# Kernel tuning notes

Hardware: AMD Instinct MI355X
Metric: run time of the kernel (lower is better)

## Reference

```python
import jax, jax.numpy as jnp
import numpy as np

RES = 128          # voxel grid resolution
N = 262144
C_IN = 64
C_OUT = 64
K = 3              # kernel size -> 27 offsets


def _build_rulebook(coords, res, k):
    """Submanifold sparse conv rulebook (stride=1, padding=k//2).
    Returns in_idx, out_idx [K^3, N] int32 and mask [K^3, N] float32."""
    n = coords.shape[0]
    lin = (coords[:, 0] * res + coords[:, 1]) * res + coords[:, 2]
    order = np.argsort(lin)
    sorted_lin = lin[order]
    r = k // 2
    in_idx, out_idx, mask = [], [], []
    for dx in range(-r, r + 1):
        for dy in range(-r, r + 1):
            for dz in range(-r, r + 1):
                nb = coords + np.array([dx, dy, dz])
                inb = np.all((nb >= 0) & (nb < res), axis=1)
                nlin = (nb[:, 0] * res + nb[:, 1]) * res + nb[:, 2]
                pos = np.searchsorted(sorted_lin, nlin)
                pos_c = np.clip(pos, 0, n - 1)
                found = inb & (sorted_lin[pos_c] == nlin)
                in_idx.append(np.where(found, order[pos_c], 0))
                out_idx.append(np.where(found, np.arange(n), 0))
                mask.append(found.astype(np.float32))
    return (np.asarray(in_idx, np.int32), np.asarray(out_idx, np.int32),
            np.asarray(mask, np.float32))


def setup_inputs() -> dict:
    rng = np.random.default_rng(0)
    lin = rng.choice(RES ** 3, size=N, replace=False)
    coords = np.stack([lin // (RES * RES), (lin // RES) % RES, lin % RES], axis=1)
    in_idx, out_idx, mask = _build_rulebook(coords, RES, K)

    key = jax.random.key(0)
    kf, kw, kb = jax.random.split(key, 3)
    feats = jax.random.normal(kf, (N, C_IN), dtype=jnp.float32)
    weight = jax.random.normal(kw, (K ** 3, C_IN, C_OUT), dtype=jnp.float32) * 0.02
    bias = jax.random.normal(kb, (C_OUT,), dtype=jnp.float32) * 0.02
    return {
        "feats": feats,
        "weight": weight,
        "bias": bias,
        "in_idx": jnp.asarray(in_idx),
        "out_idx": jnp.asarray(out_idx),
        "mask": jnp.asarray(mask),
    }


def reference(feats, weight, bias, in_idx, out_idx, mask):
    # gather -> GEMM -> scatter per kernel offset (27 fixed offsets)
    n = feats.shape[0]
    out = jnp.tile(bias[None, :], (n, 1))  # [N, C_out]
    for k in range(weight.shape[0]):
        g = feats[in_idx[k]] * mask[k][:, None]   # [N, C_in], zeros where no pair
        out = out.at[out_idx[k]].add(g @ weight[k])  # invalid rows add zeros at row 0
    return out
```

## Files before the change

### kernel.cpp

```cpp
#include <hip/hip_runtime.h>

#define CIN  64
#define COUT 64
#define KVOL 27

typedef __attribute__((ext_vector_type(8))) short bf16x8;
typedef __attribute__((ext_vector_type(4))) float f32x4;

union U4H8 { uint4 u; bf16x8 h; };

static __device__ __forceinline__ unsigned short f2bf(float x) {
    union { float f; unsigned int u; } v; v.f = x;
    return (unsigned short)((v.u + 0x7FFFu + ((v.u >> 16) & 1u)) >> 16);
}

__global__ __launch_bounds__(256) void pack_w(const float* __restrict__ W,
                                              unsigned short* __restrict__ wf) {
    int t = blockIdx.x * 256 + threadIdx.x;
    if (t >= KVOL * 8 * 64) return;
    int lane  = t & 63;
    int frag  = (t >> 6) & 7;
    int k     = t >> 9;
    int kh    = frag >> 2, nt = frag & 3;
    int col   = nt * 16 + (lane & 15);
    int kbase = kh * 32 + (lane >> 4) * 8;
    const float* src = W + (size_t)k * (CIN * COUT) + (size_t)kbase * COUT + col;
    unsigned int pk[4];
    #pragma unroll
    for (int j = 0; j < 4; ++j) {
        unsigned int lo = f2bf(src[(2 * j) * COUT]);
        unsigned int hi = f2bf(src[(2 * j + 1) * COUT]);
        pk[j] = lo | (hi << 16);
    }
    *reinterpret_cast<uint4*>(wf + (size_t)t * 8) = make_uint4(pk[0], pk[1], pk[2], pk[3]);
}

__global__ __launch_bounds__(256) void cvt_feats(const float* __restrict__ f,
                                                 uint4* __restrict__ o, int total8) {
    int t = blockIdx.x * 256 + threadIdx.x;
    if (t < total8) {
        const float4* p = reinterpret_cast<const float4*>(f) + 2 * (size_t)t;
        float4 a = p[0], b = p[1];
        unsigned int u0 = (unsigned int)f2bf(a.x) | ((unsigned int)f2bf(a.y) << 16);
        unsigned int u1 = (unsigned int)f2bf(a.z) | ((unsigned int)f2bf(a.w) << 16);
        unsigned int u2 = (unsigned int)f2bf(b.x) | ((unsigned int)f2bf(b.y) << 16);
        unsigned int u3 = (unsigned int)f2bf(b.z) | ((unsigned int)f2bf(b.w) << 16);
        o[t] = make_uint4(u0, u1, u2, u3);
    } else if (t < total8 + 8) {
        o[t] = make_uint4(0u, 0u, 0u, 0u);
    }
}

__global__ __launch_bounds__(128) void spconv_mfma64(
    const char* __restrict__ fbf,
    const uint4* __restrict__ wf4,
    const float* __restrict__ bias,
    const int*   __restrict__ in_idx,
    const float* __restrict__ mask,
    float* __restrict__ out, int n)
{
    const int tid  = threadIdx.x;
    const int lane = tid & 63;
    const int wv   = tid >> 6;
    const int rloc = lane & 15;
    const int grp  = lane >> 4;
    const int row0 = blockIdx.x * 128 + wv * 64;

    __shared__ uint4 lds_w[2][512];

    f32x4 acc[4][4];
    #pragma unroll
    for (int nt = 0; nt < 4; ++nt) {
        float b = bias[nt * 16 + rloc];
        f32x4 v = {b, b, b, b};
        acc[0][nt] = v; acc[1][nt] = v; acc[2][nt] = v; acc[3][nt] = v;
    }

    int rowt[4];
    #pragma unroll
    for (int t = 0; t < 4; ++t) rowt[t] = row0 + 16 * t + rloc;

    const unsigned zoff = (unsigned)n * 128u;

    int idxb[4]; float mskb[4];
    #pragma unroll
    for (int t = 0; t < 4; ++t) { idxb[t] = in_idx[rowt[t]]; mskb[t] = mask[rowt[t]]; }

    unsigned offs[2][4];
    #pragma unroll
    for (int t = 0; t < 4; ++t)
        offs[0][t] = (mskb[t] != 0.0f) ? (unsigned)idxb[t] * 128u : zoff;

    #pragma unroll
    for (int t = 0; t < 4; ++t) {
        idxb[t] = in_idx[(size_t)n + rowt[t]];
        mskb[t] = mask[(size_t)n + rowt[t]];
    }

    U4H8 a[2][4][2];
    #pragma unroll
    for (int t = 0; t < 4; ++t) {
        const uint4* p = reinterpret_cast<const uint4*>(fbf + offs[0][t]) + grp;
        a[0][t][0].u = p[0];
        a[0][t][1].u = p[4];
    }

    lds_w[0][tid]       = wf4[tid];
    lds_w[0][tid + 128] = wf4[tid + 128];
    lds_w[0][tid + 256] = wf4[tid + 256];
    lds_w[0][tid + 384] = wf4[tid + 384];
    __syncthreads();

    #pragma unroll
    for (int k = 0; k < KVOL; ++k) {
        const int cur = k & 1;
        const int nxt = cur ^ 1;

        uint4 w0, w1, w2, w3;
        if (k + 1 < KVOL) {
            const uint4* s = wf4 + (size_t)(k + 1) * 512;
            w0 = s[tid]; w1 = s[tid + 128]; w2 = s[tid + 256]; w3 = s[tid + 384];
        }

        if (k + 1 < KVOL) {
            #pragma unroll
            for (int t = 0; t < 4; ++t)
                offs[nxt][t] = (mskb[t] != 0.0f) ? (unsigned)idxb[t] * 128u : zoff;
        }

        if (k + 2 < KVOL) {
            const size_t kb = (size_t)(k + 2) * n;
            #pragma unroll
            for (int t = 0; t < 4; ++t) {
                idxb[t] = in_idx[kb + rowt[t]];
                mskb[t] = mask[kb + rowt[t]];
            }
        }

        if (k + 1 < KVOL) {
            #pragma unroll
            for (int t = 0; t < 4; ++t) {
                const uint4* p = reinterpret_cast<const uint4*>(fbf + offs[nxt][t]) + grp;
                a[nxt][t][0].u = p[0];
                a[nxt][t][1].u = p[4];
            }
        }

        U4H8 bf[2][4];
        #pragma unroll
        for (int kh = 0; kh < 2; ++kh)
            #pragma unroll
            for (int ntl = 0; ntl < 4; ++ntl)
                bf[kh][ntl].u = lds_w[cur][(kh * 4 + ntl) * 64 + lane];

        #pragma unroll
        for (int t = 0; t < 4; ++t)
            #pragma unroll
            for (int ntl = 0; ntl < 4; ++ntl) {
                acc[t][ntl] = __builtin_amdgcn_mfma_f32_16x16x32_bf16(a[cur][t][0].h, bf[0][ntl].h, acc[t][ntl], 0, 0, 0);
                acc[t][ntl] = __builtin_amdgcn_mfma_f32_16x16x32_bf16(a[cur][t][1].h, bf[1][ntl].h, acc[t][ntl], 0, 0, 0);
            }

        if (k + 1 < KVOL) {
            lds_w[nxt][tid]       = w0;
            lds_w[nxt][tid + 128] = w1;
            lds_w[nxt][tid + 256] = w2;
            lds_w[nxt][tid + 384] = w3;
            __syncthreads();
        }
    }

    #pragma unroll
    for (int t = 0; t < 4; ++t)
        #pragma unroll
        for (int ntl = 0; ntl < 4; ++ntl)
            #pragma unroll
            for (int r = 0; r < 4; ++r) {
                int orow = row0 + 16 * t + grp * 4 + r;
                out[(size_t)orow * COUT + ntl * 16 + rloc] = acc[t][ntl][r];
            }
}

static __device__ __forceinline__ bf16x8 cvt8(float4 a, float4 b, float m) {
    bf16x8 r;
    r[0] = (short)f2bf(a.x * m); r[1] = (short)f2bf(a.y * m);
    r[2] = (short)f2bf(a.z * m); r[3] = (short)f2bf(a.w * m);
    r[4] = (short)f2bf(b.x * m); r[5] = (short)f2bf(b.y * m);
    r[6] = (short)f2bf(b.z * m); r[7] = (short)f2bf(b.w * m);
    return r;
}

__global__ __launch_bounds__(256) void spconv_mfma_f32(
    const float* __restrict__ feats,
    const unsigned short* __restrict__ wf,
    const float* __restrict__ bias,
    const int*   __restrict__ in_idx,
    const float* __restrict__ mask,
    float* __restrict__ out, int n)
{
    const int tid  = threadIdx.x;
    const int lane = tid & 63;
    const int wv   = tid >> 6;
    const int rloc = lane & 15;
    const int grp  = lane >> 4;
    const int row0 = blockIdx.x * 128 + wv * 32;

    __shared__ uint4 lds_w[2][512];

    f32x4 acc[2][4];
    #pragma unroll
    for (int nt = 0; nt < 4; ++nt) {
        float b = bias[nt * 16 + rloc];
        f32x4 v = {b, b, b, b};
        acc[0][nt] = v; acc[1][nt] = v;
    }

    const uint4* wf4 = reinterpret_cast<const uint4*>(wf);
    lds_w[0][tid]       = wf4[tid];
    lds_w[0][tid + 256] = wf4[tid + 256];
    __syncthreads();

    const int rowA = row0 + rloc;
    const int rowB = rowA + 16;

    for (int koff = 0; koff < KVOL; ++koff) {
        const int cur = koff & 1;
        uint4 w0, w1;
        const bool pf = (koff + 1 < KVOL);
        if (pf) {
            const uint4* s = wf4 + (size_t)(koff + 1) * 512;
            w0 = s[tid]; w1 = s[tid + 256];
        }

        const size_t kb = (size_t)koff * n;
        const int   idxA = in_idx[kb + rowA];
        const float mA   = mask[kb + rowA];
        const int   idxB = in_idx[kb + rowB];
        const float mB   = mask[kb + rowB];

        const float4* fA = reinterpret_cast<const float4*>(feats + (size_t)idxA * CIN + grp * 8);
        const float4* fB = reinterpret_cast<const float4*>(feats + (size_t)idxB * CIN + grp * 8);
        float4 a0 = fA[0], a1 = fA[1], a2 = fA[8], a3 = fA[9];
        float4 c0 = fB[0], c1 = fB[1], c2 = fB[8], c3 = fB[9];

        bf16x8 aA0 = cvt8(a0, a1, mA), aA1 = cvt8(a2, a3, mA);
        bf16x8 aB0 = cvt8(c0, c1, mB), aB1 = cvt8(c2, c3, mB);

        U4H8 bf[2][4];
        #pragma unroll
        for (int kh = 0; kh < 2; ++kh)
            #pragma unroll
            for (int nt = 0; nt < 4; ++nt)
                bf[kh][nt].u = lds_w[cur][(kh * 4 + nt) * 64 + lane];

        #pragma unroll
        for (int nt = 0; nt < 4; ++nt) {
            acc[0][nt] = __builtin_amdgcn_mfma_f32_16x16x32_bf16(aA0, bf[0][nt].h, acc[0][nt], 0, 0, 0);
            acc[0][nt] = __builtin_amdgcn_mfma_f32_16x16x32_bf16(aA1, bf[1][nt].h, acc[0][nt], 0, 0, 0);
            acc[1][nt] = __builtin_amdgcn_mfma_f32_16x16x32_bf16(aB0, bf[0][nt].h, acc[1][nt], 0, 0, 0);
            acc[1][nt] = __builtin_amdgcn_mfma_f32_16x16x32_bf16(aB1, bf[1][nt].h, acc[1][nt], 0, 0, 0);
        }

        if (pf) {
            lds_w[cur ^ 1][tid]       = w0;
            lds_w[cur ^ 1][tid + 256] = w1;
        }
        __syncthreads();
    }

    #pragma unroll
    for (int t = 0; t < 2; ++t)
        #pragma unroll
        for (int nt = 0; nt < 4; ++nt)
            #pragma unroll
            for (int r = 0; r < 4; ++r) {
                int orow = row0 + t * 16 + grp * 4 + r;
                out[(size_t)orow * COUT + nt * 16 + rloc] = acc[t][nt][r];
            }
}

extern "C" void kernel_launch(void* const* d_in, const int* in_sizes, int n_in,
                              void* d_out, int out_size, void* d_ws, size_t ws_size,
                              hipStream_t stream)
{
    const float* feats  = (const float*)d_in[0];
    const float* weight = (const float*)d_in[1];
    const float* bias   = (const float*)d_in[2];
    const int*   in_idx = (const int*)  d_in[3];
    const float* mask   = (const float*)d_in[5];
    float* out = (float*)d_out;

    const int n = in_sizes[0] / CIN;

    const size_t WF_BYTES  = (size_t)KVOL * 8 * 64 * 16;
    const size_t FBF_BYTES = (size_t)(n + 1) * CIN * 2;

    unsigned short* wf = (unsigned short*)d_ws;
    const int packN = KVOL * 8 * 64;
    pack_w<<<(packN + 255) / 256, 256, 0, stream>>>(weight, wf);

    if (ws_size >= WF_BYTES + FBF_BYTES) {
        char* fbf = (char*)d_ws + WF_BYTES;
        const int total8 = n * 8;
        cvt_feats<<<(total8 + 8 + 255) / 256, 256, 0, stream>>>(feats, (uint4*)fbf, total8);
        spconv_mfma64<<<n / 128, 128, 0, stream>>>(fbf, (const uint4*)wf, bias,
                                                   in_idx, mask, out, n);
    } else {
        spconv_mfma_f32<<<n / 128, 256, 0, stream>>>(feats, wf, bias,
                                                     in_idx, mask, out, n);
    }
}
```

Before: 99.13 us.

## Split output channels across waves and load weights directly from global memory

Each block now covers 64 rows with 4 waves, and each wave computes one 16-column slice of the output instead of all 64 columns. Weight fragments are read per wave straight from global memory (L2-cached) and double-buffered in registers, which removes the LDS staging and the per-offset __syncthreads. Index and mask prefetching moves one stage further ahead. In exchange every wave gathers the same feature rows, so gather traffic per output row is four times higher (relying on cache hits), but there are fewer accumulators per thread and likely higher occupancy.

```diff
diff --git a/kernel.cpp b/kernel.cpp
--- a/kernel.cpp
+++ b/kernel.cpp
@@ -51,7 +51,7 @@
     }
 }
 
-__global__ __launch_bounds__(128) void spconv_mfma64(
+__global__ __launch_bounds__(256) void spconv_nsplit(
     const char* __restrict__ fbf,
     const uint4* __restrict__ wf4,
     const float* __restrict__ bias,
@@ -64,16 +64,13 @@
     const int wv   = tid >> 6;
     const int rloc = lane & 15;
     const int grp  = lane >> 4;
-    const int row0 = blockIdx.x * 128 + wv * 64;
-
-    __shared__ uint4 lds_w[2][512];
-
-    f32x4 acc[4][4];
-    #pragma unroll
-    for (int nt = 0; nt < 4; ++nt) {
-        float b = bias[nt * 16 + rloc];
-        f32x4 v = {b, b, b, b};
-        acc[0][nt] = v; acc[1][nt] = v; acc[2][nt] = v; acc[3][nt] = v;
+    const int row0 = blockIdx.x * 64;
+
+    f32x4 acc[4];
+    {
+        const float bb = bias[wv * 16 + rloc];
+        f32x4 v = {bb, bb, bb, bb};
+        acc[0] = v; acc[1] = v; acc[2] = v; acc[3] = v;
     }
 
     int rowt[4];
@@ -82,103 +79,77 @@
 
     const unsigned zoff = (unsigned)n * 128u;
 
-    int idxb[4]; float mskb[4];
-    #pragma unroll
-    for (int t = 0; t < 4; ++t) { idxb[t] = in_idx[rowt[t]]; mskb[t] = mask[rowt[t]]; }
-
-    unsigned offs[2][4];
-    #pragma unroll
-    for (int t = 0; t < 4; ++t)
-        offs[0][t] = (mskb[t] != 0.0f) ? (unsigned)idxb[t] * 128u : zoff;
-
+    int idxb[2][4]; float mskb[2][4];
+    #pragma unroll
+    for (int t = 0; t < 4; ++t) { idxb[0][t] = in_idx[rowt[t]];            mskb[0][t] = mask[rowt[t]]; }
+    #pragma unroll
+    for (int t = 0; t < 4; ++t) { idxb[1][t] = in_idx[(size_t)n + rowt[t]]; mskb[1][t] = mask[(size_t)n + rowt[t]]; }
+
+    U4H8 a[2][4][2];
+    U4H8 b[2][2];
+    {
+        unsigned o[4];
+        #pragma unroll
+        for (int t = 0; t < 4; ++t)
+            o[t] = (mskb[0][t] != 0.0f) ? (unsigned)idxb[0][t] * 128u : zoff;
+        #pragma unroll
+        for (int t = 0; t < 4; ++t) {
+            const uint4* p = reinterpret_cast<const uint4*>(fbf + o[t]) + grp;
+            a[0][t][0].u = p[0];
+            a[0][t][1].u = p[4];
+        }
+        b[0][0].u = wf4[(0 * 8 + 0 * 4 + wv) * 64 + lane];
+        b[0][1].u = wf4[(0 * 8 + 1 * 4 + wv) * 64 + lane];
+    }
     #pragma unroll
     for (int t = 0; t < 4; ++t) {
-        idxb[t] = in_idx[(size_t)n + rowt[t]];
-        mskb[t] = mask[(size_t)n + rowt[t]];
-    }
-
-    U4H8 a[2][4][2];
-    #pragma unroll
-    for (int t = 0; t < 4; ++t) {
-        const uint4* p = reinterpret_cast<const uint4*>(fbf + offs[0][t]) + grp;
-        a[0][t][0].u = p[0];
-        a[0][t][1].u = p[4];
-    }
-
-    lds_w[0][tid]       = wf4[tid];
-    lds_w[0][tid + 128] = wf4[tid + 128];
-    lds_w[0][tid + 256] = wf4[tid + 256];
-    lds_w[0][tid + 384] = wf4[tid + 384];
-    __syncthreads();
+        idxb[0][t] = in_idx[(size_t)2 * n + rowt[t]];
+        mskb[0][t] = mask[(size_t)2 * n + rowt[t]];
+    }
 
     #pragma unroll
     for (int k = 0; k < KVOL; ++k) {
         const int cur = k & 1;
         const int nxt = cur ^ 1;
 
-        uint4 w0, w1, w2, w3;
         if (k + 1 < KVOL) {
-            const uint4* s = wf4 + (size_t)(k + 1) * 512;
-            w0 = s[tid]; w1 = s[tid + 128]; w2 = s[tid + 256]; w3 = s[tid + 384];
-        }
-
-        if (k + 1 < KVOL) {
+            unsigned o[4];
             #pragma unroll
             for (int t = 0; t < 4; ++t)
-                offs[nxt][t] = (mskb[t] != 0.0f) ? (unsigned)idxb[t] * 128u : zoff;
-        }
-
-        if (k + 2 < KVOL) {
-            const size_t kb = (size_t)(k + 2) * n;
+                o[t] = (mskb[nxt][t] != 0.0f) ? (unsigned)idxb[nxt][t] * 128u : zoff;
             #pragma unroll
             for (int t = 0; t < 4; ++t) {
-                idxb[t] = in_idx[kb + rowt[t]];
-                mskb[t] = mask[kb + rowt[t]];
-            }
-        }
-
-        if (k + 1 < KVOL) {
-            #pragma unroll
-            for (int t = 0; t < 4; ++t) {
-                const uint4* p = reinterpret_cast<const uint4*>(fbf + offs[nxt][t]) + grp;
+                const uint4* p = reinterpret_cast<const uint4*>(fbf + o[t]) + grp;
                 a[nxt][t][0].u = p[0];
                 a[nxt][t][1].u = p[4];
             }
-        }
-
-        U4H8 bf[2][4];
-        #pragma unroll
-        for (int kh = 0; kh < 2; ++kh)
-            #pragma unroll
-            for (int ntl = 0; ntl < 4; ++ntl)
-                bf[kh][ntl].u = lds_w[cur][(kh * 4 + ntl) * 64 + lane];
-
-        #pragma unroll
-        for (int t = 0; t < 4; ++t)
-            #pragma unroll
-            for (int ntl = 0; ntl < 4; ++ntl) {
-                acc[t][ntl] = __builtin_amdgcn_mfma_f32_16x16x32_bf16(a[cur][t][0].h, bf[0][ntl].h, acc[t][ntl], 0, 0, 0);
-                acc[t][ntl] = __builtin_amdgcn_mfma_f32_16x16x32_bf16(a[cur][t][1].h, bf[1][ntl].h, acc[t][ntl], 0, 0, 0);
+            b[nxt][0].u = wf4[((k + 1) * 8 + wv) * 64 + lane];
+            b[nxt][1].u = wf4[((k + 1) * 8 + 4 + wv) * 64 + lane];
+        }
+
+        if (k + 3 < KVOL) {
+            const size_t kb = (size_t)(k + 3) * n;
+            #pragma unroll
+            for (int t = 0; t < 4; ++t) {
+                idxb[nxt][t] = in_idx[kb + rowt[t]];
+                mskb[nxt][t] = mask[kb + rowt[t]];
             }
-
-        if (k + 1 < KVOL) {
-            lds_w[nxt][tid]       = w0;
-            lds_w[nxt][tid + 128] = w1;
-            lds_w[nxt][tid + 256] = w2;
-            lds_w[nxt][tid + 384] = w3;
-            __syncthreads();
+        }
+
+        #pragma unroll
+        for (int t = 0; t < 4; ++t) {
+            acc[t] = __builtin_amdgcn_mfma_f32_16x16x32_bf16(a[cur][t][0].h, b[cur][0].h, acc[t], 0, 0, 0);
+            acc[t] = __builtin_amdgcn_mfma_f32_16x16x32_bf16(a[cur][t][1].h, b[cur][1].h, acc[t], 0, 0, 0);
         }
     }
 
     #pragma unroll
     for (int t = 0; t < 4; ++t)
         #pragma unroll
-        for (int ntl = 0; ntl < 4; ++ntl)
-            #pragma unroll
-            for (int r = 0; r < 4; ++r) {
-                int orow = row0 + 16 * t + grp * 4 + r;
-                out[(size_t)orow * COUT + ntl * 16 + rloc] = acc[t][ntl][r];
-            }
+        for (int r = 0; r < 4; ++r) {
+            int orow = row0 + 16 * t + grp * 4 + r;
+            out[(size_t)orow * COUT + wv * 16 + rloc] = acc[t][r];
+        }
 }
 
 static __device__ __forceinline__ bf16x8 cvt8(float4 a, float4 b, float m) {
@@ -303,8 +274,8 @@
         char* fbf = (char*)d_ws + WF_BYTES;
         const int total8 = n * 8;
         cvt_feats<<<(total8 + 8 + 255) / 256, 256, 0, stream>>>(feats, (uint4*)fbf, total8);
-        spconv_mfma64<<<n / 128, 128, 0, stream>>>(fbf, (const uint4*)wf, bias,
-                                                   in_idx, mask, out, n);
+        spconv_nsplit<<<n / 64, 256, 0, stream>>>(fbf, (const uint4*)wf, bias,
+                                                  in_idx, mask, out, n);
     } else {
         spconv_mfma_f32<<<n / 128, 256, 0, stream>>>(feats, wf, bias,
                                                      in_idx, mask, out, n);
```

New measurement: 228.4 us. +130.4%, slower.

## Drop LDS weight staging and barriers, read weights from global per wave

Applied to the files above, without the earlier changes.

The sparse-conv MFMA kernel no longer stages each offset's weights in double-buffered LDS with a __syncthreads per offset. Each wave now loads its weight fragments straight from global memory, which should hit in cache because all blocks share the same small packed weight buffer. Blocks grow to 256 threads and block IDs are remapped in chunks of eight, presumably to group neighbouring rows per XCD for L2 locality. The explicit prefetch of the next offset's gathered features is removed, so gather latency now depends on the compiler and wave interleaving to hide it.

```diff
diff --git a/kernel.cpp b/kernel.cpp
--- a/kernel.cpp
+++ b/kernel.cpp
@@ -51,7 +51,7 @@
     }
 }
 
-__global__ __launch_bounds__(128) void spconv_mfma64(
+__global__ __launch_bounds__(256) void spconv_nobar(
     const char* __restrict__ fbf,
     const uint4* __restrict__ wf4,
     const float* __restrict__ bias,
@@ -64,9 +64,14 @@
     const int wv   = tid >> 6;
     const int rloc = lane & 15;
     const int grp  = lane >> 4;
-    const int row0 = blockIdx.x * 128 + wv * 64;
-
-    __shared__ uint4 lds_w[2][512];
+
+    const int nwg = gridDim.x;
+    int bid = blockIdx.x;
+    if ((nwg & 7) == 0) {
+        const int chunk = nwg >> 3;
+        bid = (blockIdx.x & 7) * chunk + (blockIdx.x >> 3);
+    }
+    const int row0 = bid * 256 + wv * 64;
 
     f32x4 acc[4][4];
     #pragma unroll
@@ -82,67 +87,34 @@
 
     const unsigned zoff = (unsigned)n * 128u;
 
-    int idxb[4]; float mskb[4];
-    #pragma unroll
-    for (int t = 0; t < 4; ++t) { idxb[t] = in_idx[rowt[t]]; mskb[t] = mask[rowt[t]]; }
-
-    unsigned offs[2][4];
-    #pragma unroll
-    for (int t = 0; t < 4; ++t)
-        offs[0][t] = (mskb[t] != 0.0f) ? (unsigned)idxb[t] * 128u : zoff;
-
-    #pragma unroll
-    for (int t = 0; t < 4; ++t) {
-        idxb[t] = in_idx[(size_t)n + rowt[t]];
-        mskb[t] = mask[(size_t)n + rowt[t]];
-    }
-
-    U4H8 a[2][4][2];
-    #pragma unroll
-    for (int t = 0; t < 4; ++t) {
-        const uint4* p = reinterpret_cast<const uint4*>(fbf + offs[0][t]) + grp;
-        a[0][t][0].u = p[0];
-        a[0][t][1].u = p[4];
-    }
-
-    lds_w[0][tid]       = wf4[tid];
-    lds_w[0][tid + 128] = wf4[tid + 128];
-    lds_w[0][tid + 256] = wf4[tid + 256];
-    lds_w[0][tid + 384] = wf4[tid + 384];
-    __syncthreads();
+    int idxb[2][4]; float mskb[2][4];
+    #pragma unroll
+    for (int t = 0; t < 4; ++t) { idxb[0][t] = in_idx[rowt[t]];             mskb[0][t] = mask[rowt[t]]; }
+    #pragma unroll
+    for (int t = 0; t < 4; ++t) { idxb[1][t] = in_idx[(size_t)n + rowt[t]]; mskb[1][t] = mask[(size_t)n + rowt[t]]; }
 
     #pragma unroll
     for (int k = 0; k < KVOL; ++k) {
-        const int cur = k & 1;
-        const int nxt = cur ^ 1;
-
-        uint4 w0, w1, w2, w3;
-        if (k + 1 < KVOL) {
-            const uint4* s = wf4 + (size_t)(k + 1) * 512;
-            w0 = s[tid]; w1 = s[tid + 128]; w2 = s[tid + 256]; w3 = s[tid + 384];
-        }
-
-        if (k + 1 < KVOL) {
-            #pragma unroll
-            for (int t = 0; t < 4; ++t)
-                offs[nxt][t] = (mskb[t] != 0.0f) ? (unsigned)idxb[t] * 128u : zoff;
+        const int slot = k & 1;
+
+        unsigned o[4];
+        #pragma unroll
+        for (int t = 0; t < 4; ++t)
+            o[t] = (mskb[slot][t] != 0.0f) ? (unsigned)idxb[slot][t] * 128u : zoff;
+        U4H8 af[4][2];
+        #pragma unroll
+        for (int t = 0; t < 4; ++t) {
+            const uint4* p = reinterpret_cast<const uint4*>(fbf + o[t]) + grp;
+            af[t][0].u = p[0];
+            af[t][1].u = p[4];
         }
 
         if (k + 2 < KVOL) {
             const size_t kb = (size_t)(k + 2) * n;
             #pragma unroll
             for (int t = 0; t < 4; ++t) {
-                idxb[t] = in_idx[kb + rowt[t]];
-                mskb[t] = mask[kb + rowt[t]];
-            }
-        }
-
-        if (k + 1 < KVOL) {
-            #pragma unroll
-            for (int t = 0; t < 4; ++t) {
-                const uint4* p = reinterpret_cast<const uint4*>(fbf + offs[nxt][t]) + grp;
-                a[nxt][t][0].u = p[0];
-                a[nxt][t][1].u = p[4];
+                idxb[slot][t] = in_idx[kb + rowt[t]];
+                mskb[slot][t] = mask[kb + rowt[t]];
             }
         }
 
@@ -151,23 +123,15 @@
         for (int kh = 0; kh < 2; ++kh)
             #pragma unroll
             for (int ntl = 0; ntl < 4; ++ntl)
-                bf[kh][ntl].u = lds_w[cur][(kh * 4 + ntl) * 64 + lane];
+                bf[kh][ntl].u = wf4[((size_t)k * 8 + kh * 4 + ntl) * 64 + lane];
 
         #pragma unroll
         for (int t = 0; t < 4; ++t)
             #pragma unroll
             for (int ntl = 0; ntl < 4; ++ntl) {
-                acc[t][ntl] = __builtin_amdgcn_mfma_f32_16x16x32_bf16(a[cur][t][0].h, bf[0][ntl].h, acc[t][ntl], 0, 0, 0);
-                acc[t][ntl] = __builtin_amdgcn_mfma_f32_16x16x32_bf16(a[cur][t][1].h, bf[1][ntl].h, acc[t][ntl], 0, 0, 0);
-            }
-
-        if (k + 1 < KVOL) {
-            lds_w[nxt][tid]       = w0;
-            lds_w[nxt][tid + 128] = w1;
-            lds_w[nxt][tid + 256] = w2;
-            lds_w[nxt][tid + 384] = w3;
-            __syncthreads();
-        }
+                acc[t][ntl] = __builtin_amdgcn_mfma_f32_16x16x32_bf16(af[t][0].h, bf[0][ntl].h, acc[t][ntl], 0, 0, 0);
+                acc[t][ntl] = __builtin_amdgcn_mfma_f32_16x16x32_bf16(af[t][1].h, bf[1][ntl].h, acc[t][ntl], 0, 0, 0);
+            }
     }
 
     #pragma unroll
@@ -303,8 +267,8 @@
         char* fbf = (char*)d_ws + WF_BYTES;
         const int total8 = n * 8;
         cvt_feats<<<(total8 + 8 + 255) / 256, 256, 0, stream>>>(feats, (uint4*)fbf, total8);
-        spconv_mfma64<<<n / 128, 128, 0, stream>>>(fbf, (const uint4*)wf, bias,
-                                                   in_idx, mask, out, n);
+        spconv_nobar<<<n / 256, 256, 0, stream>>>(fbf, (const uint4*)wf, bias,
+                                                  in_idx, mask, out, n);
     } else {
         spconv_mfma_f32<<<n / 128, 256, 0, stream>>>(feats, wf, bias,
                                                      in_idx, mask, out, n);
```

New measurement: 139.0 us. 40.2% more time.
